# Optimization experiments

Measured on AMD Instinct MI355X. Metric: run time of the kernel, lower is better.

The kernel has to match this reference:

```python
import jax, jax.numpy as jnp
import numpy as np

LEAK = 0.1
K = 16  # nsample

def leaky(x):
    return jnp.where(x > 0, x, LEAK * x)

def setup_inputs() -> dict:
    key = jax.random.key(0)
    ks = jax.random.split(key, 16)
    B, N, C, D = 2, 8192, 128, 128
    s = 0.05
    return {
        "xyz1": jax.random.normal(ks[0], (B, 3, N), jnp.float32),
        "xyz2": jax.random.normal(ks[1], (B, 3, N), jnp.float32),
        "points1": jax.random.normal(ks[2], (B, C, N), jnp.float32),
        "points2": jax.random.normal(ks[3], (B, C, N), jnp.float32),
        "W_t11": jax.random.normal(ks[4], (D, C), jnp.float32) * s,
        "b_t11": jax.random.normal(ks[5], (D,), jnp.float32) * s,
        "W_t22": jax.random.normal(ks[6], (D, C), jnp.float32) * s,
        "b_t22": jax.random.normal(ks[7], (D,), jnp.float32) * s,
        "W_pos": jax.random.normal(ks[8], (D, 3), jnp.float32) * s,
        "b_pos": jax.random.normal(ks[9], (D,), jnp.float32) * s,
        "W_mlp1": jax.random.normal(ks[10], (D, D), jnp.float32) * s,
        "b_mlp1": jax.random.normal(ks[11], (D,), jnp.float32) * s,
        "W_mlp2": jax.random.normal(ks[12], (D, D), jnp.float32) * s,
        "b_mlp2": jax.random.normal(ks[13], (D,), jnp.float32) * s,
    }

def reference(xyz1, xyz2, points1, points2,
              W_t11, b_t11, W_t22, b_t22, W_pos, b_pos,
              W_mlp1, b_mlp1, W_mlp2, b_mlp2):
    # xyz*: [B,3,N], points*: [B,C,N]
    x1 = jnp.transpose(xyz1, (0, 2, 1))  # [B,N1,3]
    x2 = jnp.transpose(xyz2, (0, 2, 1))  # [B,N2,3]
    # 1x1 conv1d (t11/t22) -> [B,N,D]
    p1 = jnp.einsum('dc,bcn->bnd', W_t11, points1) + b_t11
    p2 = jnp.einsum('dc,bcn->bnd', W_t22, points2) + b_t22
    # squared distances [B,N1,N2]
    dist = (jnp.sum(x1 ** 2, -1)[:, :, None]
            + jnp.sum(x2 ** 2, -1)[:, None, :]
            - 2.0 * jnp.einsum('bnc,bmc->bnm', x1, x2))
    _, idx = jax.lax.top_k(-dist, K)  # [B,N1,K] nearest neighbors
    gather = jax.vmap(lambda pts, ix: pts[ix])  # per-batch fancy index
    nbr_xyz = gather(x2, idx)   # [B,N1,K,3]
    g2 = gather(p2, idx)        # [B,N1,K,D]
    direction = nbr_xyz - x1[:, :, None, :]
    pos = jnp.einsum('dc,bnkc->bnkd', W_pos, direction) + b_pos
    new_pts = leaky(g2 + p1[:, :, None, :] + pos)  # BN is Identity (use_bn=False)
    new_pts = leaky(jnp.einsum('dc,bnkc->bnkd', W_mlp1, new_pts) + b_mlp1)
    new_pts = leaky(jnp.einsum('dc,bnkc->bnkd', W_mlp2, new_pts) + b_mlp2)
    out = jnp.max(new_pts, axis=2)  # max over nsample -> [B,N1,D]
    return jnp.transpose(out, (0, 2, 1))  # [B,D,N1] like torch
```

## Files before the change

kernel.cpp:

```cpp
#include <hip/hip_runtime.h>
#include <hip/hip_bf16.h>

static constexpr int B_ = 2;
static constexpr int N_ = 8192;
static constexpr int C_ = 128;
static constexpr int D_ = 128;
static constexpr int K_ = 16;

typedef float f32x4 __attribute__((ext_vector_type(4)));
typedef short s16x8 __attribute__((ext_vector_type(8)));

__device__ __forceinline__ float lrelu(float x) { return fmaxf(x, 0.1f * x); }
__device__ __forceinline__ unsigned short f2bf(float f) {
  __hip_bfloat16 h = __float2bfloat16(f);
  unsigned short u;
  __builtin_memcpy(&u, &h, 2);
  return u;
}
__device__ __forceinline__ float bfl(unsigned int u) { return __uint_as_float(u << 16); }
__device__ __forceinline__ float bfh(unsigned int u) { return __uint_as_float(u & 0xffff0000u); }
__device__ __forceinline__ float rfl(float v) {
  return __uint_as_float((unsigned int)__builtin_amdgcn_readfirstlane((int)__float_as_uint(v)));
}

__global__ __launch_bounds__(256) void prep_kernel(
    const float* __restrict__ Wt11, const float* __restrict__ Wt22,
    const float* __restrict__ Wm1, const float* __restrict__ Wm2,
    const float* __restrict__ Wpos, const float* __restrict__ xyz2,
    const float* __restrict__ bt11, const float* __restrict__ bpos,
    float* __restrict__ Wt1T, float* __restrict__ Wt2T,
    unsigned short* __restrict__ w1bf, unsigned short* __restrict__ w2bf,
    float* __restrict__ wpx, float* __restrict__ wpy, float* __restrict__ wpz,
    float* __restrict__ b1c, f32x4* __restrict__ cand4) {
  int i = blockIdx.x * 256 + threadIdx.x;
  if (i < C_ * D_) {
    int d = i >> 7, c = i & 127;
    Wt1T[c * D_ + d] = Wt11[i];
    Wt2T[c * D_ + d] = Wt22[i];
    w1bf[i] = f2bf(Wm1[i]);
    w2bf[i] = f2bf(Wm2[i]);
    if (i < D_) {
      wpx[i] = Wpos[i * 3 + 0];
      wpy[i] = Wpos[i * 3 + 1];
      wpz[i] = Wpos[i * 3 + 2];
      b1c[i] = bt11[i] + bpos[i];
    }
    int bb = i >> 13, m = i & 8191;
    const float* s2 = xyz2 + (size_t)bb * 3 * N_;
    float x = s2[m], y = s2[N_ + m], z = s2[2 * N_ + m];
    f32x4 c4;
    c4[0] = -x; c4[1] = -y; c4[2] = -z;
    c4[3] = 0.5f * (x * x + y * y + z * z);
    cand4[(size_t)bb * N_ + m] = c4;
  }
}

__device__ __forceinline__ void conv_body(
    char* smem, int cbid,
    const float* __restrict__ pts, const float* __restrict__ WT,
    const float* __restrict__ bias, unsigned short* __restrict__ dst) {
  float (*tile)[64] = (float(*)[64])smem;
  int b = cbid >> 7;
  int n0 = (cbid & 127) << 6;
  int t = threadIdx.x;
  const float* src = pts + (size_t)b * C_ * N_ + n0;
  for (int i = t; i < C_ * 64; i += 256) {
    int c = i >> 6, nl = i & 63;
    tile[c][nl] = src[(size_t)c * N_ + nl];
  }
  __syncthreads();
  int w = t >> 6, lane = t & 63;
  int d0 = w * 32;
  float acc[32];
#pragma unroll
  for (int j = 0; j < 32; ++j) acc[j] = 0.f;
  for (int c = 0; c < C_; ++c) {
    float x = tile[c][lane];
    const f32x4* wp = (const f32x4*)(WT + c * D_ + d0);
#pragma unroll
    for (int j = 0; j < 8; ++j) {
      f32x4 wv = wp[j];
#pragma unroll
      for (int q = 0; q < 4; ++q) acc[4 * j + q] += wv[q] * x;
    }
  }
  unsigned short* drow = dst + ((size_t)(b * N_ + n0 + lane)) * D_ + d0;
#pragma unroll
  for (int j8 = 0; j8 < 4; ++j8) {
    uint4 ov;
    unsigned int us[8];
#pragma unroll
    for (int e = 0; e < 8; ++e)
      us[e] = f2bf(acc[8 * j8 + e] + bias[d0 + 8 * j8 + e]);
    ov.x = us[0] | (us[1] << 16);
    ov.y = us[2] | (us[3] << 16);
    ov.z = us[4] | (us[5] << 16);
    ov.w = us[6] | (us[7] << 16);
    *(uint4*)(drow + 8 * j8) = ov;
  }
}

__device__ __forceinline__ void knn_body(
    char* smem, int kbid,
    const float* __restrict__ xyz1, const f32x4* __restrict__ cand4,
    int* __restrict__ idx_out) {
  unsigned int (*idxbuf)[8][128] = (unsigned int(*)[8][128])smem;
  unsigned long long (*keybuf)[128] = (unsigned long long(*)[128])(smem + 16384);
  unsigned int (*icnt)[8] = (unsigned int(*)[8])(smem + 20480);

  int b = kbid >> 8;
  int q0 = (kbid & 255) << 5;
  int t = threadIdx.x;
  int w = t >> 6, lane = t & 63;
  int qbase = q0 + (w << 3);

  const float* s1 = xyz1 + (size_t)b * 3 * N_;
  const f32x4* cb = cand4 + (size_t)b * N_;

  if (lane < 8) icnt[w][lane] = 0u;

  float qx[8], qy[8], qz[8], dmin[8];
#pragma unroll
  for (int qq = 0; qq < 8; ++qq) {
    int q = qbase + qq;
    qx[qq] = rfl(s1[q]);
    qy[qq] = rfl(s1[N_ + q]);
    qz[qq] = rfl(s1[2 * N_ + q]);
    dmin[qq] = 1e30f;
  }

  {
    f32x4 p0 = cb[lane], p1 = cb[64 + lane], p2 = cb[128 + lane], p3 = cb[192 + lane];
    auto proc1 = [&](f32x4 c) {
#pragma unroll
      for (int qq = 0; qq < 8; ++qq) {
        float s = __builtin_fmaf(c[0], qx[qq],
                  __builtin_fmaf(c[1], qy[qq],
                  __builtin_fmaf(c[2], qz[qq], c[3])));
        dmin[qq] = fminf(dmin[qq], s);
      }
    };
    for (int i = 0; i < 124; i += 4) {
      f32x4 c0 = p0; p0 = cb[((i + 4) << 6) + lane]; proc1(c0);
      f32x4 c1 = p1; p1 = cb[((i + 5) << 6) + lane]; proc1(c1);
      f32x4 c2 = p2; p2 = cb[((i + 6) << 6) + lane]; proc1(c2);
      f32x4 c3 = p3; p3 = cb[((i + 7) << 6) + lane]; proc1(c3);
    }
    proc1(p0); proc1(p1); proc1(p2); proc1(p3);
  }

  float thr[8];
#pragma unroll 1
  for (int qq = 0; qq < 8; ++qq) {
    unsigned int ukey = __float_as_uint(dmin[qq]);
    ukey ^= ((unsigned int)(((int)ukey) >> 31)) | 0x80000000u;
    unsigned int sel = 0;
    for (int bit = 31; bit >= 0; --bit) {
      unsigned int trial = sel | (1u << bit);
      int c_lt = __popcll(__ballot(ukey < trial));
      sel = (c_lt < 16) ? trial : sel;
    }
    unsigned int su = sel ^ ((sel & 0x80000000u) ? 0x80000000u : 0xFFFFFFFFu);
    float tf = __uint_as_float(su);
    thr[qq] = tf + (1e-4f + 4e-7f * fabsf(tf));
  }

  {
    f32x4 p0 = cb[lane], p1 = cb[64 + lane], p2 = cb[128 + lane], p3 = cb[192 + lane];
    auto proc2 = [&](f32x4 c, int m) {
#pragma unroll
      for (int qq = 0; qq < 8; ++qq) {
        float s = __builtin_fmaf(c[0], qx[qq],
                  __builtin_fmaf(c[1], qy[qq],
                  __builtin_fmaf(c[2], qz[qq], c[3])));
        if (s <= thr[qq]) {
          unsigned int pos = atomicAdd(&icnt[w][qq], 1u);
          if (pos < 128u) idxbuf[w][qq][pos] = (unsigned int)m;
        }
      }
    };
    for (int i = 0; i < 124; i += 4) {
      f32x4 c0 = p0; p0 = cb[((i + 4) << 6) + lane]; proc2(c0, (i << 6) + lane);
      f32x4 c1 = p1; p1 = cb[((i + 5) << 6) + lane]; proc2(c1, ((i + 1) << 6) + lane);
      f32x4 c2 = p2; p2 = cb[((i + 6) << 6) + lane]; proc2(c2, ((i + 2) << 6) + lane);
      f32x4 c3 = p3; p3 = cb[((i + 7) << 6) + lane]; proc2(c3, ((i + 3) << 6) + lane);
    }
    proc2(p0, (124 << 6) + lane);
    proc2(p1, (125 << 6) + lane);
    proc2(p2, (126 << 6) + lane);
    proc2(p3, (127 << 6) + lane);
  }

#pragma unroll 1
  for (int qq = 0; qq < 8; ++qq) {
    int Cq = (int)icnt[w][qq];
    if (Cq > 128) Cq = 128;
    bool v0 = lane < Cq;
    unsigned int i0v = v0 ? idxbuf[w][qq][lane] : 0u;
    f32x4 c0 = cb[i0v];
    float t0x = c0[0] + qx[qq], t0y = c0[1] + qy[qq], t0z = c0[2] + qz[qq];
    float d0 = __builtin_fmaf(t0x, t0x, __builtin_fmaf(t0y, t0y, t0z * t0z));
    unsigned long long key0 =
        v0 ? ((((unsigned long long)__float_as_uint(d0)) << 13) | i0v) : ~0ull;
    unsigned long long key1 = ~0ull;
    unsigned int i1v = 0;
    if (Cq > 64) {
      bool v1 = (lane + 64) < Cq;
      i1v = v1 ? idxbuf[w][qq][lane + 64] : 0u;
      f32x4 c1 = cb[i1v];
      float t1x = c1[0] + qx[qq], t1y = c1[1] + qy[qq], t1z = c1[2] + qz[qq];
      float d1 = __builtin_fmaf(t1x, t1x, __builtin_fmaf(t1y, t1y, t1z * t1z));
      key1 = v1 ? ((((unsigned long long)__float_as_uint(d1)) << 13) | i1v) : ~0ull;
    }
    keybuf[w][lane] = key0;
    keybuf[w][lane + 64] = key1;
    int rank0 = 0, rank1 = 0;
    for (int j = 0; j < Cq; ++j) {
      unsigned long long kj = keybuf[w][j];
      rank0 += (kj < key0) ? 1 : 0;
      rank1 += (kj < key1) ? 1 : 0;
    }
    int* dst = idx_out + (((size_t)b * N_ + (qbase + qq)) << 4);
    if (v0 && rank0 < K_) dst[rank0] = (int)i0v;
    if (key1 != ~0ull && rank1 < K_) dst[rank1] = (int)i1v;
  }
}

__global__ __launch_bounds__(256, 5) void fat_kernel(
    const float* __restrict__ xyz1, const f32x4* __restrict__ cand4,
    int* __restrict__ idx_out,
    const float* __restrict__ points1, const float* __restrict__ points2,
    const float* __restrict__ Wt1T, const float* __restrict__ Wt2T,
    const float* __restrict__ b1c, const float* __restrict__ bt22,
    unsigned short* __restrict__ p1b, unsigned short* __restrict__ p2b) {
  __shared__ __align__(16) char smem[32768];
  int bid = blockIdx.x;
  if (bid < 512) {
    knn_body(smem, bid, xyz1, cand4, idx_out);
  } else if (bid < 768) {
    conv_body(smem, bid - 512, points1, Wt1T, b1c, p1b);
  } else {
    conv_body(smem, bid - 768, points2, Wt2T, bt22, p2b);
  }
}

__global__ __launch_bounds__(256, 4) void fuse_kernel(
    const float* __restrict__ xyz1, const float* __restrict__ xyz2,
    const unsigned short* __restrict__ p1b, const unsigned short* __restrict__ p2b,
    const int* __restrict__ idxb,
    const unsigned short* __restrict__ w1bf, const unsigned short* __restrict__ w2bf,
    const float* __restrict__ wpx, const float* __restrict__ wpy,
    const float* __restrict__ wpz,
    const float* __restrict__ b1, const float* __restrict__ b2,
    float* __restrict__ out) {
  __shared__ unsigned char Abuf[32768];
  __shared__ float epib[4][8][32];

  int bid = blockIdx.x;
  int b = bid >> 10;
  int n0 = (bid & 1023) << 3;
  int t = threadIdx.x;
  int wv = t >> 6, lane = t & 63;
  int lrow = lane & 15, lk = lane >> 4;

  s16x8 wfr[2][4];
#pragma unroll
  for (int j2 = 0; j2 < 2; ++j2)
#pragma unroll
    for (int ks = 0; ks < 4; ++ks) {
      int row = wv * 32 + j2 * 16 + lrow;
      wfr[j2][ks] = *(const s16x8*)(w1bf + row * D_ + ks * 32 + lk * 8);
    }

  {
    int row = t >> 1, half = t & 1;
    int nl = row >> 4, kn = row & 15;
    int n = n0 + nl;
    int j = idxb[(((size_t)b * N_ + n) << 4) + kn];
    const float* s1 = xyz1 + (size_t)b * 3 * N_;
    const float* s2 = xyz2 + (size_t)b * 3 * N_;
    float dx = s2[j] - s1[n];
    float dy = s2[N_ + j] - s1[N_ + n];
    float dz = s2[2 * N_ + j] - s1[2 * N_ + n];
    const uint4* g2r = (const uint4*)(p2b + ((size_t)(b * N_ + j)) * D_ + half * 64);
    const uint4* p1r = (const uint4*)(p1b + ((size_t)(b * N_ + n)) * D_ + half * 64);
    int rswz = (row & 7) << 4;
#pragma unroll
    for (int it = 0; it < 8; ++it) {
      int dbase = half * 64 + it * 8;
      uint4 gv = g2r[it];
      uint4 pv = p1r[it];
      float g[8] = {bfl(gv.x), bfh(gv.x), bfl(gv.y), bfh(gv.y),
                    bfl(gv.z), bfh(gv.z), bfl(gv.w), bfh(gv.w)};
      float pp[8] = {bfl(pv.x), bfh(pv.x), bfl(pv.y), bfh(pv.y),
                     bfl(pv.z), bfh(pv.z), bfl(pv.w), bfh(pv.w)};
      f32x4 wxa = *(const f32x4*)(wpx + dbase);
      f32x4 wxb = *(const f32x4*)(wpx + dbase + 4);
      f32x4 wya = *(const f32x4*)(wpy + dbase);
      f32x4 wyb = *(const f32x4*)(wpy + dbase + 4);
      f32x4 wza = *(const f32x4*)(wpz + dbase);
      f32x4 wzb = *(const f32x4*)(wpz + dbase + 4);
      unsigned int us[8];
#pragma unroll
      for (int q = 0; q < 8; ++q) {
        float wx = q < 4 ? wxa[q] : wxb[q - 4];
        float wy = q < 4 ? wya[q] : wyb[q - 4];
        float wz = q < 4 ? wza[q] : wzb[q - 4];
        float v = __builtin_fmaf(wx, dx, __builtin_fmaf(wy, dy,
                  __builtin_fmaf(wz, dz, g[q] + pp[q])));
        us[q] = f2bf(lrelu(v));
      }
      uint4 val4;
      val4.x = us[0] | (us[1] << 16);
      val4.y = us[2] | (us[3] << 16);
      val4.z = us[4] | (us[5] << 16);
      val4.w = us[6] | (us[7] << 16);
      int off = (row << 8) + (dbase << 1);
      *(uint4*)(Abuf + (off ^ rswz)) = val4;
    }
  }
  __syncthreads();

  const f32x4 fzero = {0.f, 0.f, 0.f, 0.f};
  f32x4 acc[8][2];
#pragma unroll
  for (int m = 0; m < 8; ++m) { acc[m][0] = fzero; acc[m][1] = fzero; }

#pragma unroll
  for (int ks = 0; ks < 4; ++ks) {
#pragma unroll
    for (int m = 0; m < 8; ++m) {
      int rw = m * 16 + lrow;
      int off = (rw << 8) + (ks << 6) + (lk << 4);
      s16x8 afr = *(const s16x8*)(Abuf + (off ^ ((rw & 7) << 4)));
      acc[m][0] = __builtin_amdgcn_mfma_f32_16x16x32_bf16(afr, wfr[0][ks], acc[m][0], 0, 0, 0);
      acc[m][1] = __builtin_amdgcn_mfma_f32_16x16x32_bf16(afr, wfr[1][ks], acc[m][1], 0, 0, 0);
    }
  }
  __syncthreads();

#pragma unroll
  for (int j2 = 0; j2 < 2; ++j2)
#pragma unroll
    for (int ks = 0; ks < 4; ++ks) {
      int row = wv * 32 + j2 * 16 + lrow;
      wfr[j2][ks] = *(const s16x8*)(w2bf + row * D_ + ks * 32 + lk * 8);
    }

  {
    float bias1[2];
    bias1[0] = b1[wv * 32 + lrow];
    bias1[1] = b1[wv * 32 + 16 + lrow];
#pragma unroll
    for (int m = 0; m < 8; ++m)
#pragma unroll
      for (int j2 = 0; j2 < 2; ++j2)
#pragma unroll
        for (int r = 0; r < 4; ++r) {
          int rw = m * 16 + lk * 4 + r;
          int col = wv * 32 + j2 * 16 + lrow;
          unsigned short hv = f2bf(lrelu(acc[m][j2][r] + bias1[j2]));
          int off = (rw << 8) + (col << 1);
          *(unsigned short*)(Abuf + (off ^ ((rw & 7) << 4))) = hv;
        }
  }
  __syncthreads();

#pragma unroll
  for (int m = 0; m < 8; ++m) { acc[m][0] = fzero; acc[m][1] = fzero; }

#pragma unroll
  for (int ks = 0; ks < 4; ++ks) {
#pragma unroll
    for (int m = 0; m < 8; ++m) {
      int rw = m * 16 + lrow;
      int off = (rw << 8) + (ks << 6) + (lk << 4);
      s16x8 afr = *(const s16x8*)(Abuf + (off ^ ((rw & 7) << 4)));
      acc[m][0] = __builtin_amdgcn_mfma_f32_16x16x32_bf16(afr, wfr[0][ks], acc[m][0], 0, 0, 0);
      acc[m][1] = __builtin_amdgcn_mfma_f32_16x16x32_bf16(afr, wfr[1][ks], acc[m][1], 0, 0, 0);
    }
  }

  float bias2[2];
  bias2[0] = b2[wv * 32 + lrow];
  bias2[1] = b2[wv * 32 + 16 + lrow];
#pragma unroll
  for (int m = 0; m < 8; ++m) {
#pragma unroll
    for (int j2 = 0; j2 < 2; ++j2) {
      float mx = -1e30f;
#pragma unroll
      for (int r = 0; r < 4; ++r) mx = fmaxf(mx, lrelu(acc[m][j2][r] + bias2[j2]));
      mx = fmaxf(mx, __shfl_xor(mx, 16, 64));
      mx = fmaxf(mx, __shfl_xor(mx, 32, 64));
      if (lk == 0) epib[wv][m][j2 * 16 + lrow] = mx;
    }
  }
  {
    int dl = lane >> 1, nh = lane & 1;
    f32x4 o;
#pragma unroll
    for (int i2 = 0; i2 < 4; ++i2) o[i2] = epib[wv][nh * 4 + i2][dl];
    *(f32x4*)(out + ((size_t)(b * D_ + wv * 32 + dl)) * N_ + n0 + nh * 4) = o;
  }
}

extern "C" void kernel_launch(void* const* d_in, const int* in_sizes, int n_in,
                              void* d_out, int out_size, void* d_ws, size_t ws_size,
                              hipStream_t stream) {
  (void)in_sizes; (void)n_in; (void)out_size; (void)ws_size;
  const float* xyz1    = (const float*)d_in[0];
  const float* xyz2    = (const float*)d_in[1];
  const float* points1 = (const float*)d_in[2];
  const float* points2 = (const float*)d_in[3];
  const float* W_t11   = (const float*)d_in[4];
  const float* b_t11   = (const float*)d_in[5];
  const float* W_t22   = (const float*)d_in[6];
  const float* b_t22   = (const float*)d_in[7];
  const float* W_pos   = (const float*)d_in[8];
  const float* b_pos   = (const float*)d_in[9];
  const float* W_mlp1  = (const float*)d_in[10];
  const float* b_mlp1  = (const float*)d_in[11];
  const float* W_mlp2  = (const float*)d_in[12];
  const float* b_mlp2  = (const float*)d_in[13];
  float* out = (float*)d_out;

  char* ws = (char*)d_ws;
  unsigned short* p1b  = (unsigned short*)(ws);
  unsigned short* p2b  = (unsigned short*)(ws + 4194304);
  float* Wt1T          = (float*)(ws + 8388608);
  float* Wt2T          = (float*)(ws + 8454144);
  unsigned short* w1bf = (unsigned short*)(ws + 8519680);
  unsigned short* w2bf = (unsigned short*)(ws + 8552448);
  float* wpx           = (float*)(ws + 8585216);
  float* wpy           = (float*)(ws + 8585728);
  float* wpz           = (float*)(ws + 8586240);
  f32x4* cand4         = (f32x4*)(ws + 8586752);
  int* idxws           = (int*)(ws + 8848896);
  float* b1c           = (float*)(ws + 9897472);

  prep_kernel<<<64, 256, 0, stream>>>(W_t11, W_t22, W_mlp1, W_mlp2, W_pos, xyz2,
                                      b_t11, b_pos,
                                      Wt1T, Wt2T, w1bf, w2bf, wpx, wpy, wpz,
                                      b1c, cand4);
  fat_kernel<<<1024, 256, 0, stream>>>(xyz1, cand4, idxws,
                                       points1, points2, Wt1T, Wt2T,
                                       b1c, b_t22, p1b, p2b);
  fuse_kernel<<<B_ * 1024, 256, 0, stream>>>(xyz1, xyz2, p1b, p2b, idxws,
                                             w1bf, w2bf, wpx, wpy, wpz,
                                             b_mlp1, b_mlp2, out);
}
```

Baseline: 159.4 us.

## Halve per-block work in KNN and conv, pack FMAs into float2, raise occupancy

The KNN blocks now handle 4 queries per wave instead of 8, and the conv blocks handle 32 points instead of 64, with each lane computing 16 output channels. The grid doubles to 2048 blocks, shared memory halves, and launch bounds rise to 8 blocks per CU, so more waves are resident for latency hiding. The KNN distance FMAs and mins are written on float2 vectors so the compiler can emit packed FP32 instructions. In exchange, every candidate point is now read from cand4 twice as many times in total, since each wave scans all candidates for fewer queries.

```diff
diff --git a/kernel.cpp b/kernel.cpp
--- a/kernel.cpp
+++ b/kernel.cpp
@@ -8,6 +8,7 @@
 static constexpr int K_ = 16;
 
 typedef float f32x4 __attribute__((ext_vector_type(4)));
+typedef float f32x2 __attribute__((ext_vector_type(2)));
 typedef short s16x8 __attribute__((ext_vector_type(8)));
 
 __device__ __forceinline__ float lrelu(float x) { return fmaxf(x, 0.1f * x); }
@@ -21,6 +22,20 @@
 __device__ __forceinline__ float bfh(unsigned int u) { return __uint_as_float(u & 0xffff0000u); }
 __device__ __forceinline__ float rfl(float v) {
   return __uint_as_float((unsigned int)__builtin_amdgcn_readfirstlane((int)__float_as_uint(v)));
+}
+__device__ __forceinline__ f32x2 fma2(f32x2 a, f32x2 b, f32x2 c) {
+#if __has_builtin(__builtin_elementwise_fma)
+  return __builtin_elementwise_fma(a, b, c);
+#else
+  f32x2 r; r[0] = __builtin_fmaf(a[0], b[0], c[0]); r[1] = __builtin_fmaf(a[1], b[1], c[1]); return r;
+#endif
+}
+__device__ __forceinline__ f32x2 min2(f32x2 a, f32x2 b) {
+#if __has_builtin(__builtin_elementwise_min)
+  return __builtin_elementwise_min(a, b);
+#else
+  f32x2 r; r[0] = fminf(a[0], b[0]); r[1] = fminf(a[1], b[1]); return r;
+#endif
 }
 
 __global__ __launch_bounds__(256) void prep_kernel(
@@ -59,34 +74,35 @@
     char* smem, int cbid,
     const float* __restrict__ pts, const float* __restrict__ WT,
     const float* __restrict__ bias, unsigned short* __restrict__ dst) {
-  float (*tile)[64] = (float(*)[64])smem;
-  int b = cbid >> 7;
-  int n0 = (cbid & 127) << 6;
+  float (*tile)[32] = (float(*)[32])smem;
+  int b = cbid >> 8;
+  int n0 = (cbid & 255) << 5;
   int t = threadIdx.x;
   const float* src = pts + (size_t)b * C_ * N_ + n0;
-  for (int i = t; i < C_ * 64; i += 256) {
-    int c = i >> 6, nl = i & 63;
+  for (int i = t; i < C_ * 32; i += 256) {
+    int c = i >> 5, nl = i & 31;
     tile[c][nl] = src[(size_t)c * N_ + nl];
   }
   __syncthreads();
   int w = t >> 6, lane = t & 63;
-  int d0 = w * 32;
-  float acc[32];
-#pragma unroll
-  for (int j = 0; j < 32; ++j) acc[j] = 0.f;
+  int nl = lane & 31;
+  int d0 = w * 32 + (lane >> 5) * 16;
+  float acc[16];
+#pragma unroll
+  for (int j = 0; j < 16; ++j) acc[j] = 0.f;
   for (int c = 0; c < C_; ++c) {
-    float x = tile[c][lane];
+    float x = tile[c][nl];
     const f32x4* wp = (const f32x4*)(WT + c * D_ + d0);
 #pragma unroll
-    for (int j = 0; j < 8; ++j) {
+    for (int j = 0; j < 4; ++j) {
       f32x4 wv = wp[j];
 #pragma unroll
       for (int q = 0; q < 4; ++q) acc[4 * j + q] += wv[q] * x;
     }
   }
-  unsigned short* drow = dst + ((size_t)(b * N_ + n0 + lane)) * D_ + d0;
-#pragma unroll
-  for (int j8 = 0; j8 < 4; ++j8) {
+  unsigned short* drow = dst + ((size_t)(b * N_ + n0 + nl)) * D_ + d0;
+#pragma unroll
+  for (int j8 = 0; j8 < 2; ++j8) {
     uint4 ov;
     unsigned int us[8];
 #pragma unroll
@@ -104,40 +120,47 @@
     char* smem, int kbid,
     const float* __restrict__ xyz1, const f32x4* __restrict__ cand4,
     int* __restrict__ idx_out) {
-  unsigned int (*idxbuf)[8][128] = (unsigned int(*)[8][128])smem;
-  unsigned long long (*keybuf)[128] = (unsigned long long(*)[128])(smem + 16384);
-  unsigned int (*icnt)[8] = (unsigned int(*)[8])(smem + 20480);
-
-  int b = kbid >> 8;
-  int q0 = (kbid & 255) << 5;
+  unsigned int (*idxbuf)[4][128] = (unsigned int(*)[4][128])smem;
+  unsigned long long (*keybuf)[128] = (unsigned long long(*)[128])(smem + 8192);
+  unsigned int (*icnt)[4] = (unsigned int(*)[4])(smem + 12288);
+
+  int b = kbid >> 9;
+  int q0 = (kbid & 511) << 4;
   int t = threadIdx.x;
   int w = t >> 6, lane = t & 63;
-  int qbase = q0 + (w << 3);
+  int qbase = q0 + (w << 2);
 
   const float* s1 = xyz1 + (size_t)b * 3 * N_;
   const f32x4* cb = cand4 + (size_t)b * N_;
 
-  if (lane < 8) icnt[w][lane] = 0u;
-
-  float qx[8], qy[8], qz[8], dmin[8];
-#pragma unroll
-  for (int qq = 0; qq < 8; ++qq) {
+  if (lane < 4) icnt[w][lane] = 0u;
+
+  float qx[4], qy[4], qz[4];
+  f32x2 qxp[2], qyp[2], qzp[2], dmin2[2];
+#pragma unroll
+  for (int qq = 0; qq < 4; ++qq) {
     int q = qbase + qq;
     qx[qq] = rfl(s1[q]);
     qy[qq] = rfl(s1[N_ + q]);
     qz[qq] = rfl(s1[2 * N_ + q]);
-    dmin[qq] = 1e30f;
+  }
+#pragma unroll
+  for (int p = 0; p < 2; ++p) {
+    qxp[p] = (f32x2){qx[2 * p], qx[2 * p + 1]};
+    qyp[p] = (f32x2){qy[2 * p], qy[2 * p + 1]};
+    qzp[p] = (f32x2){qz[2 * p], qz[2 * p + 1]};
+    dmin2[p] = (f32x2){1e30f, 1e30f};
   }
 
   {
     f32x4 p0 = cb[lane], p1 = cb[64 + lane], p2 = cb[128 + lane], p3 = cb[192 + lane];
     auto proc1 = [&](f32x4 c) {
-#pragma unroll
-      for (int qq = 0; qq < 8; ++qq) {
-        float s = __builtin_fmaf(c[0], qx[qq],
-                  __builtin_fmaf(c[1], qy[qq],
-                  __builtin_fmaf(c[2], qz[qq], c[3])));
-        dmin[qq] = fminf(dmin[qq], s);
+      f32x2 cx = (f32x2){c[0], c[0]}, cy = (f32x2){c[1], c[1]};
+      f32x2 cz = (f32x2){c[2], c[2]}, cw = (f32x2){c[3], c[3]};
+#pragma unroll
+      for (int p = 0; p < 2; ++p) {
+        f32x2 s = fma2(cx, qxp[p], fma2(cy, qyp[p], fma2(cz, qzp[p], cw)));
+        dmin2[p] = min2(dmin2[p], s);
       }
     };
     for (int i = 0; i < 124; i += 4) {
@@ -149,10 +172,11 @@
     proc1(p0); proc1(p1); proc1(p2); proc1(p3);
   }
 
-  float thr[8];
+  float thr[4];
 #pragma unroll 1
-  for (int qq = 0; qq < 8; ++qq) {
-    unsigned int ukey = __float_as_uint(dmin[qq]);
+  for (int qq = 0; qq < 4; ++qq) {
+    float dm = dmin2[qq >> 1][qq & 1];
+    unsigned int ukey = __float_as_uint(dm);
     ukey ^= ((unsigned int)(((int)ukey) >> 31)) | 0x80000000u;
     unsigned int sel = 0;
     for (int bit = 31; bit >= 0; --bit) {
@@ -168,14 +192,18 @@
   {
     f32x4 p0 = cb[lane], p1 = cb[64 + lane], p2 = cb[128 + lane], p3 = cb[192 + lane];
     auto proc2 = [&](f32x4 c, int m) {
-#pragma unroll
-      for (int qq = 0; qq < 8; ++qq) {
-        float s = __builtin_fmaf(c[0], qx[qq],
-                  __builtin_fmaf(c[1], qy[qq],
-                  __builtin_fmaf(c[2], qz[qq], c[3])));
-        if (s <= thr[qq]) {
-          unsigned int pos = atomicAdd(&icnt[w][qq], 1u);
-          if (pos < 128u) idxbuf[w][qq][pos] = (unsigned int)m;
+      f32x2 cx = (f32x2){c[0], c[0]}, cy = (f32x2){c[1], c[1]};
+      f32x2 cz = (f32x2){c[2], c[2]}, cw = (f32x2){c[3], c[3]};
+#pragma unroll
+      for (int p = 0; p < 2; ++p) {
+        f32x2 s = fma2(cx, qxp[p], fma2(cy, qyp[p], fma2(cz, qzp[p], cw)));
+#pragma unroll
+        for (int h = 0; h < 2; ++h) {
+          int qq = 2 * p + h;
+          if (s[h] <= thr[qq]) {
+            unsigned int pos = atomicAdd(&icnt[w][qq], 1u);
+            if (pos < 128u) idxbuf[w][qq][pos] = (unsigned int)m;
+          }
         }
       }
     };
@@ -192,7 +220,7 @@
   }
 
 #pragma unroll 1
-  for (int qq = 0; qq < 8; ++qq) {
+  for (int qq = 0; qq < 4; ++qq) {
     int Cq = (int)icnt[w][qq];
     if (Cq > 128) Cq = 128;
     bool v0 = lane < Cq;
@@ -226,21 +254,21 @@
   }
 }
 
-__global__ __launch_bounds__(256, 5) void fat_kernel(
+__global__ __launch_bounds__(256, 8) void fat_kernel(
     const float* __restrict__ xyz1, const f32x4* __restrict__ cand4,
     int* __restrict__ idx_out,
     const float* __restrict__ points1, const float* __restrict__ points2,
     const float* __restrict__ Wt1T, const float* __restrict__ Wt2T,
     const float* __restrict__ b1c, const float* __restrict__ bt22,
     unsigned short* __restrict__ p1b, unsigned short* __restrict__ p2b) {
-  __shared__ __align__(16) char smem[32768];
+  __shared__ __align__(16) char smem[16384];
   int bid = blockIdx.x;
-  if (bid < 512) {
+  if (bid < 1024) {
     knn_body(smem, bid, xyz1, cand4, idx_out);
-  } else if (bid < 768) {
-    conv_body(smem, bid - 512, points1, Wt1T, b1c, p1b);
+  } else if (bid < 1536) {
+    conv_body(smem, bid - 1024, points1, Wt1T, b1c, p1b);
   } else {
-    conv_body(smem, bid - 768, points2, Wt2T, bt22, p2b);
+    conv_body(smem, bid - 1536, points2, Wt2T, bt22, p2b);
   }
 }
 
@@ -443,7 +471,7 @@
                                       b_t11, b_pos,
                                       Wt1T, Wt2T, w1bf, w2bf, wpx, wpy, wpz,
                                       b1c, cand4);
-  fat_kernel<<<1024, 256, 0, stream>>>(xyz1, cand4, idxws,
+  fat_kernel<<<2048, 256, 0, stream>>>(xyz1, cand4, idxws,
                                        points1, points2, Wt1T, Wt2T,
                                        b1c, b_t22, p1b, p2b);
   fuse_kernel<<<B_ * 1024, 256, 0, stream>>>(xyz1, xyz2, p1b, p2b, idxws,
```

New measurement: 172.9 us. 8.5% more time.

## Split kNN candidate scan across two waves per query group and halve conv tiles

Applied to the files above, without the earlier changes.

Each group of 8 queries is now scanned by two wavefronts, each covering half of the candidate points. Their per-lane minima are shared through LDS so the radix threshold selection can combine both halves, and the final ranking is spread across all four waves. The conv blocks process 32 points instead of 64 with 16 accumulators per thread. Together these double the fat_kernel grid, shrink shared memory and raise the occupancy hint, aiming to cut per-block latency and improve latency hiding. The cost is extra block barriers, cross-wave LDS traffic and shared atomics on the candidate counters.

```diff
diff --git a/kernel.cpp b/kernel.cpp
--- a/kernel.cpp
+++ b/kernel.cpp
@@ -21,6 +21,9 @@
 __device__ __forceinline__ float bfh(unsigned int u) { return __uint_as_float(u & 0xffff0000u); }
 __device__ __forceinline__ float rfl(float v) {
   return __uint_as_float((unsigned int)__builtin_amdgcn_readfirstlane((int)__float_as_uint(v)));
+}
+__device__ __forceinline__ unsigned int mflip(unsigned int x) {
+  return x ^ (((unsigned int)(((int)x) >> 31)) | 0x80000000u);
 }
 
 __global__ __launch_bounds__(256) void prep_kernel(
@@ -59,34 +62,35 @@
     char* smem, int cbid,
     const float* __restrict__ pts, const float* __restrict__ WT,
     const float* __restrict__ bias, unsigned short* __restrict__ dst) {
-  float (*tile)[64] = (float(*)[64])smem;
-  int b = cbid >> 7;
-  int n0 = (cbid & 127) << 6;
+  float (*tile)[32] = (float(*)[32])smem;
+  int b = cbid >> 8;
+  int n0 = (cbid & 255) << 5;
   int t = threadIdx.x;
   const float* src = pts + (size_t)b * C_ * N_ + n0;
-  for (int i = t; i < C_ * 64; i += 256) {
-    int c = i >> 6, nl = i & 63;
+  for (int i = t; i < C_ * 32; i += 256) {
+    int c = i >> 5, nl = i & 31;
     tile[c][nl] = src[(size_t)c * N_ + nl];
   }
   __syncthreads();
   int w = t >> 6, lane = t & 63;
-  int d0 = w * 32;
-  float acc[32];
-#pragma unroll
-  for (int j = 0; j < 32; ++j) acc[j] = 0.f;
+  int nl = lane & 31;
+  int d0 = w * 32 + (lane >> 5) * 16;
+  float acc[16];
+#pragma unroll
+  for (int j = 0; j < 16; ++j) acc[j] = 0.f;
   for (int c = 0; c < C_; ++c) {
-    float x = tile[c][lane];
+    float x = tile[c][nl];
     const f32x4* wp = (const f32x4*)(WT + c * D_ + d0);
 #pragma unroll
-    for (int j = 0; j < 8; ++j) {
+    for (int j = 0; j < 4; ++j) {
       f32x4 wv = wp[j];
 #pragma unroll
       for (int q = 0; q < 4; ++q) acc[4 * j + q] += wv[q] * x;
     }
   }
-  unsigned short* drow = dst + ((size_t)(b * N_ + n0 + lane)) * D_ + d0;
-#pragma unroll
-  for (int j8 = 0; j8 < 4; ++j8) {
+  unsigned short* drow = dst + ((size_t)(b * N_ + n0 + nl)) * D_ + d0;
+#pragma unroll
+  for (int j8 = 0; j8 < 2; ++j8) {
     uint4 ov;
     unsigned int us[8];
 #pragma unroll
@@ -104,20 +108,23 @@
     char* smem, int kbid,
     const float* __restrict__ xyz1, const f32x4* __restrict__ cand4,
     int* __restrict__ idx_out) {
-  unsigned int (*idxbuf)[8][128] = (unsigned int(*)[8][128])smem;
-  unsigned long long (*keybuf)[128] = (unsigned long long(*)[128])(smem + 16384);
-  unsigned int (*icnt)[8] = (unsigned int(*)[8])(smem + 20480);
-
-  int b = kbid >> 8;
-  int q0 = (kbid & 255) << 5;
+  float (*dmsh)[2][8][64] = (float(*)[2][8][64])smem;
+  unsigned long long (*keybuf)[128] = (unsigned long long(*)[128])smem;
+  unsigned int (*idxbuf)[8][128] = (unsigned int(*)[8][128])(smem + 8192);
+  unsigned int (*icnt)[8] = (unsigned int(*)[8])(smem + 16384);
+
+  int b = kbid >> 9;
+  int q0 = (kbid & 511) << 4;
   int t = threadIdx.x;
   int w = t >> 6, lane = t & 63;
-  int qbase = q0 + (w << 3);
+  int g = w >> 1, h = w & 1;
+  int qbase = q0 + (g << 3);
 
   const float* s1 = xyz1 + (size_t)b * 3 * N_;
-  const f32x4* cb = cand4 + (size_t)b * N_;
-
-  if (lane < 8) icnt[w][lane] = 0u;
+  const f32x4* cbf = cand4 + (size_t)b * N_;
+  const f32x4* cb = cbf + (h << 12);
+
+  if (t < 16) icnt[t >> 3][t & 7] = 0u;
 
   float qx[8], qy[8], qz[8], dmin[8];
 #pragma unroll
@@ -140,7 +147,7 @@
         dmin[qq] = fminf(dmin[qq], s);
       }
     };
-    for (int i = 0; i < 124; i += 4) {
+    for (int i = 0; i < 60; i += 4) {
       f32x4 c0 = p0; p0 = cb[((i + 4) << 6) + lane]; proc1(c0);
       f32x4 c1 = p1; p1 = cb[((i + 5) << 6) + lane]; proc1(c1);
       f32x4 c2 = p2; p2 = cb[((i + 6) << 6) + lane]; proc1(c2);
@@ -149,15 +156,19 @@
     proc1(p0); proc1(p1); proc1(p2); proc1(p3);
   }
 
+#pragma unroll
+  for (int qq = 0; qq < 8; ++qq) dmsh[g][h][qq][lane] = dmin[qq];
+  __syncthreads();
+
   float thr[8];
 #pragma unroll 1
   for (int qq = 0; qq < 8; ++qq) {
-    unsigned int ukey = __float_as_uint(dmin[qq]);
-    ukey ^= ((unsigned int)(((int)ukey) >> 31)) | 0x80000000u;
+    unsigned int u0 = mflip(__float_as_uint(dmin[qq]));
+    unsigned int u1 = mflip(__float_as_uint(dmsh[g][1 ^ h][qq][lane]));
     unsigned int sel = 0;
     for (int bit = 31; bit >= 0; --bit) {
       unsigned int trial = sel | (1u << bit);
-      int c_lt = __popcll(__ballot(ukey < trial));
+      int c_lt = __popcll(__ballot(u0 < trial)) + __popcll(__ballot(u1 < trial));
       sel = (c_lt < 16) ? trial : sel;
     }
     unsigned int su = sel ^ ((sel & 0x80000000u) ? 0x80000000u : 0xFFFFFFFFu);
@@ -167,6 +178,7 @@
 
   {
     f32x4 p0 = cb[lane], p1 = cb[64 + lane], p2 = cb[128 + lane], p3 = cb[192 + lane];
+    int mo = (h << 12) + lane;
     auto proc2 = [&](f32x4 c, int m) {
 #pragma unroll
       for (int qq = 0; qq < 8; ++qq) {
@@ -174,31 +186,38 @@
                   __builtin_fmaf(c[1], qy[qq],
                   __builtin_fmaf(c[2], qz[qq], c[3])));
         if (s <= thr[qq]) {
-          unsigned int pos = atomicAdd(&icnt[w][qq], 1u);
-          if (pos < 128u) idxbuf[w][qq][pos] = (unsigned int)m;
+          unsigned int pos = atomicAdd(&icnt[g][qq], 1u);
+          if (pos < 128u) idxbuf[g][qq][pos] = (unsigned int)m;
         }
       }
     };
-    for (int i = 0; i < 124; i += 4) {
-      f32x4 c0 = p0; p0 = cb[((i + 4) << 6) + lane]; proc2(c0, (i << 6) + lane);
-      f32x4 c1 = p1; p1 = cb[((i + 5) << 6) + lane]; proc2(c1, ((i + 1) << 6) + lane);
-      f32x4 c2 = p2; p2 = cb[((i + 6) << 6) + lane]; proc2(c2, ((i + 2) << 6) + lane);
-      f32x4 c3 = p3; p3 = cb[((i + 7) << 6) + lane]; proc2(c3, ((i + 3) << 6) + lane);
-    }
-    proc2(p0, (124 << 6) + lane);
-    proc2(p1, (125 << 6) + lane);
-    proc2(p2, (126 << 6) + lane);
-    proc2(p3, (127 << 6) + lane);
-  }
+    for (int i = 0; i < 60; i += 4) {
+      f32x4 c0 = p0; p0 = cb[((i + 4) << 6) + lane]; proc2(c0, mo + (i << 6));
+      f32x4 c1 = p1; p1 = cb[((i + 5) << 6) + lane]; proc2(c1, mo + ((i + 1) << 6));
+      f32x4 c2 = p2; p2 = cb[((i + 6) << 6) + lane]; proc2(c2, mo + ((i + 2) << 6));
+      f32x4 c3 = p3; p3 = cb[((i + 7) << 6) + lane]; proc2(c3, mo + ((i + 3) << 6));
+    }
+    proc2(p0, mo + (60 << 6));
+    proc2(p1, mo + (61 << 6));
+    proc2(p2, mo + (62 << 6));
+    proc2(p3, mo + (63 << 6));
+  }
+  __syncthreads();
 
 #pragma unroll 1
-  for (int qq = 0; qq < 8; ++qq) {
-    int Cq = (int)icnt[w][qq];
+  for (int j = 0; j < 4; ++j) {
+    int wq = (w << 2) + j;
+    int g2 = wq >> 3, qq2 = wq & 7;
+    int q = q0 + wq;
+    float qx2 = rfl(s1[q]);
+    float qy2 = rfl(s1[N_ + q]);
+    float qz2 = rfl(s1[2 * N_ + q]);
+    int Cq = (int)icnt[g2][qq2];
     if (Cq > 128) Cq = 128;
     bool v0 = lane < Cq;
-    unsigned int i0v = v0 ? idxbuf[w][qq][lane] : 0u;
-    f32x4 c0 = cb[i0v];
-    float t0x = c0[0] + qx[qq], t0y = c0[1] + qy[qq], t0z = c0[2] + qz[qq];
+    unsigned int i0v = v0 ? idxbuf[g2][qq2][lane] : 0u;
+    f32x4 c0 = cbf[i0v];
+    float t0x = c0[0] + qx2, t0y = c0[1] + qy2, t0z = c0[2] + qz2;
     float d0 = __builtin_fmaf(t0x, t0x, __builtin_fmaf(t0y, t0y, t0z * t0z));
     unsigned long long key0 =
         v0 ? ((((unsigned long long)__float_as_uint(d0)) << 13) | i0v) : ~0ull;
@@ -206,41 +225,41 @@
     unsigned int i1v = 0;
     if (Cq > 64) {
       bool v1 = (lane + 64) < Cq;
-      i1v = v1 ? idxbuf[w][qq][lane + 64] : 0u;
-      f32x4 c1 = cb[i1v];
-      float t1x = c1[0] + qx[qq], t1y = c1[1] + qy[qq], t1z = c1[2] + qz[qq];
+      i1v = v1 ? idxbuf[g2][qq2][lane + 64] : 0u;
+      f32x4 c1 = cbf[i1v];
+      float t1x = c1[0] + qx2, t1y = c1[1] + qy2, t1z = c1[2] + qz2;
       float d1 = __builtin_fmaf(t1x, t1x, __builtin_fmaf(t1y, t1y, t1z * t1z));
       key1 = v1 ? ((((unsigned long long)__float_as_uint(d1)) << 13) | i1v) : ~0ull;
     }
     keybuf[w][lane] = key0;
     keybuf[w][lane + 64] = key1;
     int rank0 = 0, rank1 = 0;
-    for (int j = 0; j < Cq; ++j) {
-      unsigned long long kj = keybuf[w][j];
+    for (int j2 = 0; j2 < Cq; ++j2) {
+      unsigned long long kj = keybuf[w][j2];
       rank0 += (kj < key0) ? 1 : 0;
       rank1 += (kj < key1) ? 1 : 0;
     }
-    int* dst = idx_out + (((size_t)b * N_ + (qbase + qq)) << 4);
+    int* dst = idx_out + (((size_t)b * N_ + q) << 4);
     if (v0 && rank0 < K_) dst[rank0] = (int)i0v;
     if (key1 != ~0ull && rank1 < K_) dst[rank1] = (int)i1v;
   }
 }
 
-__global__ __launch_bounds__(256, 5) void fat_kernel(
+__global__ __launch_bounds__(256, 8) void fat_kernel(
     const float* __restrict__ xyz1, const f32x4* __restrict__ cand4,
     int* __restrict__ idx_out,
     const float* __restrict__ points1, const float* __restrict__ points2,
     const float* __restrict__ Wt1T, const float* __restrict__ Wt2T,
     const float* __restrict__ b1c, const float* __restrict__ bt22,
     unsigned short* __restrict__ p1b, unsigned short* __restrict__ p2b) {
-  __shared__ __align__(16) char smem[32768];
+  __shared__ __align__(16) char smem[16448];
   int bid = blockIdx.x;
-  if (bid < 512) {
+  if (bid < 1024) {
     knn_body(smem, bid, xyz1, cand4, idx_out);
-  } else if (bid < 768) {
-    conv_body(smem, bid - 512, points1, Wt1T, b1c, p1b);
+  } else if (bid < 1536) {
+    conv_body(smem, bid - 1024, points1, Wt1T, b1c, p1b);
   } else {
-    conv_body(smem, bid - 768, points2, Wt2T, bt22, p2b);
+    conv_body(smem, bid - 1536, points2, Wt2T, bt22, p2b);
   }
 }
 
@@ -443,7 +462,7 @@
                                       b_t11, b_pos,
                                       Wt1T, Wt2T, w1bf, w2bf, wpx, wpy, wpz,
                                       b1c, cand4);
-  fat_kernel<<<1024, 256, 0, stream>>>(xyz1, cand4, idxws,
+  fat_kernel<<<2048, 256, 0, stream>>>(xyz1, cand4, idxws,
                                        points1, points2, Wt1T, Wt2T,
                                        b1c, b_t22, p1b, p2b);
   fuse_kernel<<<B_ * 1024, 256, 0, stream>>>(xyz1, xyz2, p1b, p2b, idxws,
```

New measurement: 156.2 us. 2.0% less time.
